# Optimization experiments

Hardware: AMD Instinct MI355X
Metric: run time of the kernel (lower is better)

## Reference

```python
import jax, jax.numpy as jnp
import numpy as np

MAX_DISP = 48
PATCH = 3
OFFSET = 0
PAD = PATCH // 2
EPS = 1e-3


def _unfold(x, P, pad):
    # x: [B,C,H,W] -> [B,C,K2,H,W], K2 enumerated row-major over the PxP window
    B, C, H, W = x.shape
    xp = jnp.pad(x, ((0, 0), (0, 0), (pad, pad), (pad, pad)))
    return jnp.stack([xp[:, :, i:i + H, j:j + W]
                      for i in range(P) for j in range(P)], axis=2)


def _normalize(x, axes):
    # torch F.normalize: x / clamp(||x||_2, min=eps)
    n = jnp.sqrt(jnp.sum(x * x, axis=axes, keepdims=True))
    return x / jnp.maximum(n, EPS)


def setup_inputs() -> dict:
    key = jax.random.key(0)
    k1, k2, k3 = jax.random.split(key, 3)
    shp = (2, 32, 128, 416)
    return {
        "xl": jax.random.normal(k1, shp, dtype=jnp.float32),
        "xm": jax.random.normal(k2, shp, dtype=jnp.float32),
        "xr": jax.random.normal(k3, shp, dtype=jnp.float32),
    }


def reference(xl, xm, xr):
    B, C, H, W = xl.shape
    K2 = PATCH * PATCH
    scale = (C * K2) ** 0.5

    pl = _normalize(_unfold(xl, PATCH, PAD), (1, 2))  # [B,C,K2,H,W]
    pr = _normalize(_unfold(xr, PATCH, PAD), (1, 2))
    fl = _normalize(xm, (1,))                          # [B,C,H,W]

    # fl is constant over the K2 axis, so sum patches over K2 once for sim_L/sim_R
    Sl = pl.sum(axis=2)  # [B,C,H,W]
    Sr = pr.sum(axis=2)

    cL, cR, cLR = [], [], []
    for d in range(OFFSET, OFFSET + MAX_DISP):
        if d > 0:
            # shifted_l[w] = patches_l[w+d] (zero right pad); shifted_r[w] = patches_r[w-d]
            sL = jnp.einsum('bchw,bchw->bhw', fl[..., :W - d], Sl[..., d:])
            sL = jnp.pad(sL, ((0, 0), (0, 0), (0, d)))
            sR = jnp.einsum('bchw,bchw->bhw', fl[..., d:], Sr[..., :W - d])
            sR = jnp.pad(sR, ((0, 0), (0, 0), (d, 0)))
            wlr = W - 2 * d  # overlap region of the two opposite shifts
            if wlr > 0:
                sLR = jnp.einsum('bckhw,bckhw->bhw', pl[..., 2 * d:], pr[..., :wlr])
                sLR = jnp.pad(sLR, ((0, 0), (0, 0), (d, d)))
            else:
                sLR = jnp.zeros((B, H, W), xl.dtype)
        else:
            sL = jnp.einsum('bchw,bchw->bhw', fl, Sl)
            sR = jnp.einsum('bchw,bchw->bhw', fl, Sr)
            sLR = jnp.einsum('bckhw,bckhw->bhw', pl, pr)
        cL.append(sL / scale)
        cR.append(sR / scale)
        cLR.append(sLR / scale)

    cost = jnp.stack([jnp.stack(cL, 1), jnp.stack(cR, 1), jnp.stack(cLR, 1)], axis=1)
    return jnp.clip(cost, -10.0, 10.0).astype(jnp.float16)  # [B,3,D,H,W]
```

## Files before the change

### kernel.cpp

```cpp
#include <hip/hip_runtime.h>
#include <math.h>

#define B 2
#define C 32
#define H 128
#define W 416
#define D 48
#define HW (H*W)
#define CHW (C*HW)
#define EPSN 1e-3f
#define ISCALE 0.05892556509887896f
#define ESTR 36
#define LSTR 32
#define DSPE 24
#define DSPL 16
#define NZ 3

__device__ __forceinline__ float clip10(float x) {
    return fminf(fmaxf(x, -10.0f), 10.0f);
}

#define FMA4(acc, f, k, u) acc += f[4*(k)+0]*(u).x + f[4*(k)+1]*(u).y \
                               + f[4*(k)+2]*(u).z + f[4*(k)+3]*(u).w;

__global__ __launch_bounds__(256) void k_norm(const float* __restrict__ sql,
                                              const float* __restrict__ sqr,
                                              float* __restrict__ inl,
                                              float* __restrict__ inr) {
    int idx = blockIdx.x * 256 + threadIdx.x;
    if (idx >= B * HW) return;
    int b = idx / HW, hw = idx - b * HW;
    int h = hw / W, w = hw - h * W;
    float sl = 0.f, sr = 0.f;
#pragma unroll
    for (int di = -1; di <= 1; ++di) {
        int hh = h + di;
        if (hh < 0 || hh >= H) continue;
#pragma unroll
        for (int dj = -1; dj <= 1; ++dj) {
            int ww = w + dj;
            if (ww < 0 || ww >= W) continue;
            int p = b * HW + hh * W + ww;
            sl += sql[p];
            sr += sqr[p];
        }
    }
    inl[idx] = 1.0f / fmaxf(sqrtf(sl), EPSN);
    inr[idx] = 1.0f / fmaxf(sqrtf(sr), EPSN);
}

__device__ __forceinline__ void stage_row_v2(const float* __restrict__ gsrc,
                                             float* __restrict__ lds,
                                             int tid, int nthreads) {
    for (int t = tid; t < (W / 4) * C; t += nthreads) {
        int rw = t & 7;
        int cl = (t >> 3) & 7;
        int g  = t >> 6;
        int wg = g % 13;
        int ch = g / 13;
        int c  = ch * 8 + cl;
        int w4 = (wg * 8 + rw) * 4;
        float4 v = *(const float4*)(gsrc + (size_t)c * HW + w4);
        lds[(w4 + 0) * ESTR + c] = v.x;
        lds[(w4 + 1) * ESTR + c] = v.y;
        lds[(w4 + 2) * ESTR + c] = v.z;
        lds[(w4 + 3) * ESTR + c] = v.w;
    }
}

__device__ __forceinline__ void stage_row3_swz(const float* __restrict__ gsrc,
                                               float* __restrict__ lds,
                                               int h, int tid, int nthreads) {
    for (int t = tid; t < (W / 4) * C; t += nthreads) {
        int rw = t & 7;
        int cl = (t >> 3) & 7;
        int g  = t >> 6;
        int wg = g % 13;
        int ch = g / 13;
        int c  = ch * 8 + cl;
        int w4 = (wg * 8 + rw) * 4;
        const float* p = gsrc + (size_t)c * HW + w4;
        float4 v = *(const float4*)(p);
        if (h > 0) {
            float4 a = *(const float4*)(p - W);
            v.x += a.x; v.y += a.y; v.z += a.z; v.w += a.w;
        }
        if (h < H - 1) {
            float4 a = *(const float4*)(p + W);
            v.x += a.x; v.y += a.y; v.z += a.z; v.w += a.w;
        }
        int g2 = c >> 2, wd = c & 3;
        int k0 = (w4 >> 1) & 7;
        int k1 = (k0 + 1) & 7;
        lds[(w4 + 0) * LSTR + 4 * (g2 ^ k0) + wd] = v.x;
        lds[(w4 + 1) * LSTR + 4 * (g2 ^ k0) + wd] = v.y;
        lds[(w4 + 2) * LSTR + 4 * (g2 ^ k1) + wd] = v.z;
        lds[(w4 + 3) * LSTR + 4 * (g2 ^ k1) + wd] = v.w;
    }
}

__device__ __forceinline__ float dot32e(const float* __restrict__ x,
                                        const float* __restrict__ col) {
    const float4* c4 = (const float4*)col;
    float4 u0 = c4[0], u1 = c4[1], u2 = c4[2], u3 = c4[3];
    float4 u4 = c4[4], u5 = c4[5], u6 = c4[6], u7 = c4[7];
    float a = 0.f, b = 0.f;
    FMA4(a, x, 0, u0) FMA4(a, x, 1, u1) FMA4(a, x, 2, u2) FMA4(a, x, 3, u3)
    FMA4(b, x, 4, u4) FMA4(b, x, 5, u5) FMA4(b, x, 6, u6) FMA4(b, x, 7, u7)
    return a + b;
}

__device__ __forceinline__ void dot2s(const float* __restrict__ fl0,
                                      const float* __restrict__ fl1,
                                      const float4* __restrict__ c4, int ky,
                                      float& a0, float& a1) {
    float4 u0 = c4[ky],     u1 = c4[1 ^ ky], u2 = c4[2 ^ ky], u3 = c4[3 ^ ky];
    float4 u4 = c4[4 ^ ky], u5 = c4[5 ^ ky], u6 = c4[6 ^ ky], u7 = c4[7 ^ ky];
    float x0 = 0.f, x1 = 0.f, y0 = 0.f, y1 = 0.f;
    FMA4(x0, fl0, 0, u0) FMA4(x0, fl0, 1, u1) FMA4(x0, fl0, 2, u2) FMA4(x0, fl0, 3, u3)
    FMA4(x1, fl0, 4, u4) FMA4(x1, fl0, 5, u5) FMA4(x1, fl0, 6, u6) FMA4(x1, fl0, 7, u7)
    FMA4(y0, fl1, 0, u0) FMA4(y0, fl1, 1, u1) FMA4(y0, fl1, 2, u2) FMA4(y0, fl1, 3, u3)
    FMA4(y1, fl1, 4, u4) FMA4(y1, fl1, 5, u5) FMA4(y1, fl1, 6, u6) FMA4(y1, fl1, 7, u7)
    a0 = x0 + x1; a1 = y0 + y1;
}

__global__ __launch_bounds__(256, 3) void k_lr(const float* __restrict__ xm,
                                               const float* __restrict__ xl,
                                               const float* __restrict__ xr,
                                               const float* __restrict__ inl,
                                               const float* __restrict__ inr,
                                               float* __restrict__ out) {
    __shared__ float sB[W * LSTR];
    int tid = threadIdx.x;
    int bx = blockIdx.x;
    int z = bx % NZ;
    int h = bx / NZ;
    int b = blockIdx.y;
    int d0 = z * DSPL;
    bool act = tid < (W / 2);
    int w = 2 * tid;
    int bhw = b * HW + h * W;
    const float* pm = xm + (size_t)b * CHW + h * W;

    float fl0[C], fl1[C];
    if (act) {
        float am0 = 0.f, am1 = 0.f;
#pragma unroll
        for (int c = 0; c < C; ++c) {
            float2 mv = *(const float2*)(pm + (size_t)c * HW + w);
            fl0[c] = mv.x; fl1[c] = mv.y;
            am0 += mv.x * mv.x; am1 += mv.y * mv.y;
        }
        float im0 = 1.0f / fmaxf(sqrtf(am0), EPSN);
        float im1 = 1.0f / fmaxf(sqrtf(am1), EPSN);
#pragma unroll
        for (int c = 0; c < C; ++c) { fl0[c] *= im0; fl1[c] *= im1; }
    }

    stage_row3_swz(xl + (size_t)b * CHW + h * W, sB, h, tid, 256);
    __syncthreads();
    if (act) {
        float* o = out + ((size_t)b * 3 + 0) * D * HW + h * W;
        const float* inx = inl + bhw;
        float g0a = 0.f, g0b = 0.f, g1a = 0.f, g1b = 0.f, s0p = 0.f;
        float scn = 0.f;
        for (int j = 0; j <= DSPL + 2; ++j) {
            int v = w + d0 - 1 + j;
            bool ok = (v >= 0) && (v < W);
            int vc = ok ? v : 0;
            float c0, c1;
            dot2s(fl0, fl1, (const float4*)(sB + vc * LSTR), (vc >> 1) & 7, c0, c1);
            c0 = ok ? c0 : 0.f;
            c1 = ok ? c1 : 0.f;
            float sc = scn;
            int mn = w + d0 + j - 1;
            scn = (mn >= 0 && mn < W) ? inx[mn] : 0.f;
            float s0 = 0.f, s1 = 0.f;
            if (j >= 2) {
                int m = v - 1;
                if (m < W) {
                    float s = sc * ISCALE;
                    s0 = clip10((g0a + g0b + c0) * s);
                    s1 = clip10((g1a + g1b + c1) * s);
                }
                if (j >= 3) {
                    int d = d0 + j - 3;
                    *(float2*)(o + (size_t)d * HW + w) = make_float2(s0p, s1);
                }
            }
            s0p = s0;
            g0a = g0b; g0b = c0;
            g1a = g1b; g1b = c1;
        }
    }
    __syncthreads();

    stage_row3_swz(xr + (size_t)b * CHW + h * W, sB, h, tid, 256);
    __syncthreads();
    if (act) {
        float* o = out + ((size_t)b * 3 + 1) * D * HW + h * W;
        const float* inx = inr + bhw;
        float g0a = 0.f, g0b = 0.f, g1a = 0.f, g1b = 0.f, s0p = 0.f;
        float scn = 0.f;
        for (int j = 0; j <= DSPL + 2; ++j) {
            int v = w - d0 - DSPL + j;
            bool ok = (v >= 0) && (v < W);
            int vc = ok ? v : 0;
            float c0, c1;
            dot2s(fl0, fl1, (const float4*)(sB + vc * LSTR), (vc >> 1) & 7, c0, c1);
            c0 = ok ? c0 : 0.f;
            c1 = ok ? c1 : 0.f;
            float sc = scn;
            int mn = w - d0 - DSPL + j;
            scn = (mn >= 0) ? inx[mn] : 0.f;
            float s0 = 0.f, s1 = 0.f;
            if (j >= 2) {
                int m = v - 1;
                if (m >= 0) {
                    float s = sc * ISCALE;
                    s0 = clip10((g0a + g0b + c0) * s);
                    s1 = clip10((g1a + g1b + c1) * s);
                }
                if (j >= 3) {
                    int d = d0 + DSPL + 2 - j;
                    *(float2*)(o + (size_t)d * HW + w) = make_float2(s0p, s1);
                }
            }
            s0p = s0;
            g0a = g0b; g0b = c0;
            g1a = g1b; g1b = c1;
        }
    }
}

__global__ __launch_bounds__(448) void k_e(const float* __restrict__ xl,
                                           const float* __restrict__ xr,
                                           float* __restrict__ EH,
                                           float* __restrict__ sql,
                                           float* __restrict__ sqr) {
    __shared__ float sXL[W * ESTR];
    int tid = threadIdx.x;
    int h = blockIdx.x;
    int b = blockIdx.y;
    int d0 = blockIdx.z * DSPE;
    int lane = tid & 63;
    int wv = tid >> 6;
    int v = wv * 62 + lane - 1;
    bool vin = (v >= 0) && (v < W);
    const float* br = xr + (size_t)b * CHW + h * W;

    float xrv[C];
#pragma unroll
    for (int c = 0; c < C; ++c) xrv[c] = vin ? br[c * HW + v] : 0.0f;

    stage_row_v2(xl + (size_t)b * CHW + h * W, sXL, tid, 448);
    __syncthreads();

    bool wr = (lane >= 1) && (lane <= 62) && (v < W);

    if (blockIdx.z == 0) {
        float sr_ = 0.f, sl_ = 0.f;
#pragma unroll
        for (int c = 0; c < C; ++c) sr_ += xrv[c] * xrv[c];
        if (vin) {
            const float4* c4 = (const float4*)(sXL + v * ESTR);
#pragma unroll
            for (int q = 0; q < 8; ++q) {
                float4 x = c4[q];
                sl_ += x.x * x.x + x.y * x.y + x.z * x.z + x.w * x.w;
            }
        }
        if (wr) {
            sqr[b * HW + h * W + v] = sr_;
            sql[b * HW + h * W + v] = sl_;
        }
    }

    float* pe = EH + (((size_t)b * D) * H + h) * W + v;
    for (int d = d0; d < d0 + DSPE; ++d) {
        int s = 2 * d;
        float e = 0.0f;
        if (vin && v + s < W) e = dot32e(xrv, sXL + (v + s) * ESTR);
        float em = __shfl_up(e, 1);
        float ep = __shfl_down(e, 1);
        float eh = em + e + ep;
        if (wr) pe[(size_t)d * HW] = eh;
    }
}

#define DCH 12
__global__ __launch_bounds__(448) void k_lr2(const float* __restrict__ EH,
                                             const float* __restrict__ inl,
                                             const float* __restrict__ inr,
                                             float* __restrict__ out) {
    int w = threadIdx.x;
    int dc = blockIdx.x;
    int h = blockIdx.y;
    int b = blockIdx.z;
    if (w >= W) return;
    int bhw = b * HW + h * W;
    bool hm = (h > 0), hp = (h < H - 1);

    float* o = out + ((size_t)b * 3 + 2) * D * HW + h * W + w;
#pragma unroll
    for (int i = 0; i < DCH; ++i) {
        int d = dc * DCH + i;
        float r = 0.0f;
        if (w >= d && w + d < W) {
            int vc = w - d;
            const float* base = EH + ((size_t)b * D + d) * HW + vc;
            float e = base[h * W];
            if (hm) e += base[(h - 1) * W];
            if (hp) e += base[(h + 1) * W];
            float nl = inl[bhw + w + d];
            float nr = inr[bhw + vc];
            r = clip10(e * nl * nr * ISCALE);
        }
        o[(size_t)d * HW] = r;
    }
}

extern "C" void kernel_launch(void* const* d_in, const int* in_sizes, int n_in,
                              void* d_out, int out_size, void* d_ws, size_t ws_size,
                              hipStream_t stream) {
    const float* xl = (const float*)d_in[0];
    const float* xm = (const float*)d_in[1];
    const float* xr = (const float*)d_in[2];
    float* out = (float*)d_out;

    float* ws = (float*)d_ws;
    float* inl = ws;
    float* inr = inl + B * HW;
    float* sql = inr + B * HW;
    float* sqr = sql + B * HW;
    float* EH  = sqr + B * HW;

    k_e<<<dim3(H, B, 2), dim3(448), 0, stream>>>(xl, xr, EH, sql, sqr);
    k_norm<<<dim3((B * HW + 255) / 256), dim3(256), 0, stream>>>(sql, sqr, inl, inr);
    k_lr<<<dim3(NZ * H, B), dim3(256), 0, stream>>>(xm, xl, xr, inl, inr, out);
    k_lr2<<<dim3(4, H, B), dim3(448), 0, stream>>>(EH, inl, inr, out);
}
```

Baseline: 195.5 us.

## Split k_lr disparities in halves, stage inverse norms in LDS, swizzle k_lr2 blocks

k_lr now covers 24 disparities per block instead of 16 and runs on a 2-way z grid, so the xm normalisation and row staging are shared across more disparities. The per-iteration global loads of the inverse norms move into a shared-memory array, and the branchy clamp-and-select around the dot products becomes a plain conditional. k_lr2 gets a flattened grid with an XCD-style block swizzle, and the launch-bounds occupancy hint of 3 is dropped from k_lr. Fewer blocks and higher register pressure may cut occupancy and parallelism.

```diff
diff --git a/kernel.cpp b/kernel.cpp
--- a/kernel.cpp
+++ b/kernel.cpp
@@ -12,9 +12,7 @@
 #define ISCALE 0.05892556509887896f
 #define ESTR 36
 #define LSTR 32
-#define DSPE 24
-#define DSPL 16
-#define NZ 3
+#define DSPL (D / 2)
 
 __device__ __forceinline__ float clip10(float x) {
     return fminf(fmaxf(x, -10.0f), 10.0f);
@@ -124,19 +122,18 @@
     a0 = x0 + x1; a1 = y0 + y1;
 }
 
-__global__ __launch_bounds__(256, 3) void k_lr(const float* __restrict__ xm,
-                                               const float* __restrict__ xl,
-                                               const float* __restrict__ xr,
-                                               const float* __restrict__ inl,
-                                               const float* __restrict__ inr,
-                                               float* __restrict__ out) {
+__global__ __launch_bounds__(256) void k_lr(const float* __restrict__ xm,
+                                            const float* __restrict__ xl,
+                                            const float* __restrict__ xr,
+                                            const float* __restrict__ inl,
+                                            const float* __restrict__ inr,
+                                            float* __restrict__ out) {
     __shared__ float sB[W * LSTR];
+    __shared__ float sIn[W];
     int tid = threadIdx.x;
-    int bx = blockIdx.x;
-    int z = bx % NZ;
-    int h = bx / NZ;
+    int h = blockIdx.x;
     int b = blockIdx.y;
-    int d0 = z * DSPL;
+    int d0 = blockIdx.z * DSPL;
     bool act = tid < (W / 2);
     int w = 2 * tid;
     int bhw = b * HW + h * W;
@@ -155,33 +152,30 @@
         float im1 = 1.0f / fmaxf(sqrtf(am1), EPSN);
 #pragma unroll
         for (int c = 0; c < C; ++c) { fl0[c] *= im0; fl1[c] *= im1; }
+    } else {
+#pragma unroll
+        for (int c = 0; c < C; ++c) { fl0[c] = 0.f; fl1[c] = 0.f; }
     }
 
     stage_row3_swz(xl + (size_t)b * CHW + h * W, sB, h, tid, 256);
+    for (int j = tid; j < W; j += 256) sIn[j] = inl[bhw + j];
     __syncthreads();
     if (act) {
         float* o = out + ((size_t)b * 3 + 0) * D * HW + h * W;
-        const float* inx = inl + bhw;
         float g0a = 0.f, g0b = 0.f, g1a = 0.f, g1b = 0.f, s0p = 0.f;
-        float scn = 0.f;
+#pragma unroll 3
         for (int j = 0; j <= DSPL + 2; ++j) {
             int v = w + d0 - 1 + j;
-            bool ok = (v >= 0) && (v < W);
-            int vc = ok ? v : 0;
-            float c0, c1;
-            dot2s(fl0, fl1, (const float4*)(sB + vc * LSTR), (vc >> 1) & 7, c0, c1);
-            c0 = ok ? c0 : 0.f;
-            c1 = ok ? c1 : 0.f;
-            float sc = scn;
-            int mn = w + d0 + j - 1;
-            scn = (mn >= 0 && mn < W) ? inx[mn] : 0.f;
+            float c0 = 0.f, c1 = 0.f;
+            if (v >= 0 && v < W)
+                dot2s(fl0, fl1, (const float4*)(sB + v * LSTR), (v >> 1) & 7, c0, c1);
             float s0 = 0.f, s1 = 0.f;
             if (j >= 2) {
                 int m = v - 1;
                 if (m < W) {
-                    float s = sc * ISCALE;
-                    s0 = clip10((g0a + g0b + c0) * s);
-                    s1 = clip10((g1a + g1b + c1) * s);
+                    float sc = sIn[m] * ISCALE;
+                    s0 = clip10((g0a + g0b + c0) * sc);
+                    s1 = clip10((g1a + g1b + c1) * sc);
                 }
                 if (j >= 3) {
                     int d = d0 + j - 3;
@@ -196,30 +190,24 @@
     __syncthreads();
 
     stage_row3_swz(xr + (size_t)b * CHW + h * W, sB, h, tid, 256);
+    for (int j = tid; j < W; j += 256) sIn[j] = inr[bhw + j];
     __syncthreads();
     if (act) {
         float* o = out + ((size_t)b * 3 + 1) * D * HW + h * W;
-        const float* inx = inr + bhw;
         float g0a = 0.f, g0b = 0.f, g1a = 0.f, g1b = 0.f, s0p = 0.f;
-        float scn = 0.f;
+#pragma unroll 3
         for (int j = 0; j <= DSPL + 2; ++j) {
             int v = w - d0 - DSPL + j;
-            bool ok = (v >= 0) && (v < W);
-            int vc = ok ? v : 0;
-            float c0, c1;
-            dot2s(fl0, fl1, (const float4*)(sB + vc * LSTR), (vc >> 1) & 7, c0, c1);
-            c0 = ok ? c0 : 0.f;
-            c1 = ok ? c1 : 0.f;
-            float sc = scn;
-            int mn = w - d0 - DSPL + j;
-            scn = (mn >= 0) ? inx[mn] : 0.f;
+            float c0 = 0.f, c1 = 0.f;
+            if (v >= 0 && v < W)
+                dot2s(fl0, fl1, (const float4*)(sB + v * LSTR), (v >> 1) & 7, c0, c1);
             float s0 = 0.f, s1 = 0.f;
             if (j >= 2) {
                 int m = v - 1;
                 if (m >= 0) {
-                    float s = sc * ISCALE;
-                    s0 = clip10((g0a + g0b + c0) * s);
-                    s1 = clip10((g1a + g1b + c1) * s);
+                    float sc = sIn[m] * ISCALE;
+                    s0 = clip10((g0a + g0b + c0) * sc);
+                    s1 = clip10((g1a + g1b + c1) * sc);
                 }
                 if (j >= 3) {
                     int d = d0 + DSPL + 2 - j;
@@ -242,7 +230,7 @@
     int tid = threadIdx.x;
     int h = blockIdx.x;
     int b = blockIdx.y;
-    int d0 = blockIdx.z * DSPE;
+    int d0 = blockIdx.z * DSPL;
     int lane = tid & 63;
     int wv = tid >> 6;
     int v = wv * 62 + lane - 1;
@@ -277,7 +265,7 @@
     }
 
     float* pe = EH + (((size_t)b * D) * H + h) * W + v;
-    for (int d = d0; d < d0 + DSPE; ++d) {
+    for (int d = d0; d < d0 + DSPL; ++d) {
         int s = 2 * d;
         float e = 0.0f;
         if (vin && v + s < W) e = dot32e(xrv, sXL + (v + s) * ESTR);
@@ -294,9 +282,12 @@
                                              const float* __restrict__ inr,
                                              float* __restrict__ out) {
     int w = threadIdx.x;
-    int dc = blockIdx.x;
-    int h = blockIdx.y;
-    int b = blockIdx.z;
+    int lin = blockIdx.x;
+    int sw = (lin & 7) * 128 + (lin >> 3);
+    int b  = sw >> 9;
+    int r  = sw & 511;
+    int dc = r >> 7;
+    int h  = r & 127;
     if (w >= W) return;
     int bhw = b * HW + h * W;
     bool hm = (h > 0), hp = (h < H - 1);
@@ -305,7 +296,7 @@
 #pragma unroll
     for (int i = 0; i < DCH; ++i) {
         int d = dc * DCH + i;
-        float r = 0.0f;
+        float r2 = 0.0f;
         if (w >= d && w + d < W) {
             int vc = w - d;
             const float* base = EH + ((size_t)b * D + d) * HW + vc;
@@ -314,9 +305,9 @@
             if (hp) e += base[(h + 1) * W];
             float nl = inl[bhw + w + d];
             float nr = inr[bhw + vc];
-            r = clip10(e * nl * nr * ISCALE);
-        }
-        o[(size_t)d * HW] = r;
+            r2 = clip10(e * nl * nr * ISCALE);
+        }
+        o[(size_t)d * HW] = r2;
     }
 }
 
@@ -337,6 +328,6 @@
 
     k_e<<<dim3(H, B, 2), dim3(448), 0, stream>>>(xl, xr, EH, sql, sqr);
     k_norm<<<dim3((B * HW + 255) / 256), dim3(256), 0, stream>>>(sql, sqr, inl, inr);
-    k_lr<<<dim3(NZ * H, B), dim3(256), 0, stream>>>(xm, xl, xr, inl, inr, out);
-    k_lr2<<<dim3(4, H, B), dim3(448), 0, stream>>>(EH, inl, inr, out);
-}
+    k_lr<<<dim3(H, B, 2), dim3(256), 0, stream>>>(xm, xl, xr, inl, inr, out);
+    k_lr2<<<dim3(4 * H * B), dim3(448), 0, stream>>>(EH, inl, inr, out);
+}
```

Measured after the change: 167.2 us. -14.5%, faster.
